# Performance work log

Measured on AMD Instinct MI355X. Metric: run time of the kernel, lower is better.

The kernel has to match this reference:

```python
import jax, jax.numpy as jnp
import numpy as np

B, C, H, W = 4, 512, 64, 64
CQ = C // 4  # query/key channels


def setup_inputs() -> dict:
    key = jax.random.key(0)
    ks = jax.random.split(key, 8)
    s_in = 1.0 / np.sqrt(C)
    return {
        "x": jax.random.normal(ks[0], (B, C, H, W), dtype=jnp.float32),
        "Wf_w": jax.random.normal(ks[1], (CQ, C), dtype=jnp.float32) * s_in,
        "Wf_b": jax.random.normal(ks[2], (CQ,), dtype=jnp.float32) * 0.01,
        "Wh_w": jax.random.normal(ks[3], (CQ, C), dtype=jnp.float32) * s_in,
        "Wh_b": jax.random.normal(ks[4], (CQ,), dtype=jnp.float32) * 0.01,
        "Wl_w": jax.random.normal(ks[5], (C, C), dtype=jnp.float32) * s_in,
        "Wl_b": jax.random.normal(ks[6], (C,), dtype=jnp.float32) * 0.01,
        "alpha": jax.random.uniform(ks[7], (1,), dtype=jnp.float32),
    }


def reference(x, Wf_w, Wf_b, Wh_w, Wh_b, Wl_w, Wl_b, alpha):
    b, c, h, w = x.shape
    n = h * w
    xr = x.reshape(b, c, n)  # (B, C, N)
    # 1x1 convs == per-pixel linear projections
    f = jnp.einsum('oc,bcn->bon', Wf_w, xr) + Wf_b[None, :, None]  # (B, C/4, N)
    k = jnp.einsum('oc,bcn->bon', Wh_w, xr) + Wh_b[None, :, None]  # (B, C/4, N)
    v = jnp.einsum('oc,bcn->bon', Wl_w, xr) + Wl_b[None, :, None]  # (B, C,   N)
    # t[b, i, j] = <f[:, i], k[:, j]>  -> (B, N, N)
    scores = jnp.einsum('boi,boj->bij', f, k)
    att = jax.nn.softmax(scores, axis=-1)
    # out[b, c, i] = sum_j v[b, c, j] * att[b, i, j]  (bmm with att^T)
    out = jnp.einsum('bcj,bij->bci', v, att)
    out = out.reshape(b, c, h, w)
    return out * alpha[0] + x
```

## Files before the change

### kernel.cpp

```cpp
#include <hip/hip_runtime.h>
#include <hip/hip_bf16.h>

typedef _Float16 f16;
typedef _Float16 f16x4 __attribute__((ext_vector_type(4)));
typedef _Float16 f16x8 __attribute__((ext_vector_type(8)));
typedef float f32x4 __attribute__((ext_vector_type(4)));

constexpr int BATCH = 4, C = 512, CQ = 128, N = 4096;
constexpr int OALL = 768;

constexpr size_t WS_FT   = 0;
constexpr size_t WS_KT   = WS_FT   + (size_t)BATCH * N * CQ * 2;
constexpr size_t WS_V    = WS_KT   + (size_t)BATCH * N * CQ * 2;
constexpr size_t WS_WALL = WS_V    + (size_t)BATCH * C * N * 2;
constexpr size_t WS_BALL = WS_WALL + (size_t)OALL * C * 2;

__global__ void prep_weights(const float* __restrict__ Wf_w, const float* __restrict__ Wf_b,
                             const float* __restrict__ Wh_w, const float* __restrict__ Wh_b,
                             const float* __restrict__ Wl_w, const float* __restrict__ Wl_b,
                             f16* __restrict__ wall, float* __restrict__ ball) {
    int i = blockIdx.x * 256 + threadIdx.x;
    if (i < OALL * C) {
        int o = i >> 9, c = i & 511;
        float v = (o < 128) ? Wf_w[o * C + c]
                : (o < 256) ? Wh_w[(o - 128) * C + c]
                            : Wl_w[(o - 256) * C + c];
        wall[i] = (f16)v;
    }
    if (i < OALL)
        ball[i] = (i < 128) ? Wf_b[i] : (i < 256) ? Wh_b[i - 128] : Wl_b[i - 256];
}

__global__ void __launch_bounds__(512) proj_all(const float* __restrict__ x, const f16* __restrict__ wall,
                                                const float* __restrict__ ball,
                                                f16* __restrict__ ft, f16* __restrict__ kt,
                                                f16* __restrict__ v) {
    __shared__ __align__(16) f16 xl[64][72];
    const int tid = threadIdx.x;
    const int wv  = tid >> 6;
    const int lane = tid & 63;
    const int li = lane & 15, lg = lane >> 4;
    const int b  = blockIdx.x >> 6;
    const int n0 = (blockIdx.x & 63) * 64;
    const int ob = wv * 96;
    const int nn = tid & 63, cg = tid >> 6;

    f32x4 acc[6][4] = {};
    for (int ch = 0; ch < 8; ++ch) {
        __syncthreads();
        {
            const float* xs = x + ((size_t)(b * C) + ch * 64 + cg * 8) * N + n0 + nn;
#pragma unroll
            for (int r = 0; r < 8; ++r)
                xl[nn][cg * 8 + r] = (f16)xs[(size_t)r * N];
        }
        __syncthreads();
#pragma unroll
        for (int ks = 0; ks < 2; ++ks) {
            f16x8 xfr[4];
#pragma unroll
            for (int nf = 0; nf < 4; ++nf)
                xfr[nf] = *(const f16x8*)(&xl[nf * 16 + li][ks * 32 + lg * 8]);
#pragma unroll
            for (int of = 0; of < 6; ++of) {
                f16x8 wfr = *(const f16x8*)(wall + (size_t)(ob + of * 16 + li) * C + ch * 64 + ks * 32 + lg * 8);
#pragma unroll
                for (int nf = 0; nf < 4; ++nf)
                    acc[of][nf] = __builtin_amdgcn_mfma_f32_16x16x32_f16(xfr[nf], wfr, acc[of][nf], 0, 0, 0);
            }
        }
    }
#pragma unroll
    for (int of = 0; of < 6; ++of) {
        const int o = ob + of * 16 + li;
        const float bias = ball[o];
#pragma unroll
        for (int nf = 0; nf < 4; ++nf)
#pragma unroll
            for (int r = 0; r < 4; ++r) {
                const int n = n0 + nf * 16 + lg * 4 + r;
                const f16 val = (f16)(acc[of][nf][r] + bias);
                if (o < 128) {
                    ft[(size_t)(b * N + n) * CQ + o] = val;
                } else if (o < 256) {
                    const int ck = o - 128;
                    kt[(((size_t)b * (N >> 2) + (n >> 2)) * 4 + (n & 3)) * 128 + ck] = val;
                } else {
                    const int c = o - 256;
                    v[(((size_t)b * 32 + (c >> 4)) * 512 + (n >> 3)) * 128 + (c & 15) * 8 + (n & 7)] = val;
                }
            }
    }
}

__global__ void __launch_bounds__(512, 2) attn(const f16* __restrict__ ft, const f16* __restrict__ kt,
                                               const f16* __restrict__ v,
                                               const float* __restrict__ x, const float* __restrict__ alphap,
                                               float* __restrict__ out) {
    __shared__ __align__(16) f16 kbuf[2][128 * 128];
    __shared__ __align__(16) f16 pbuf[64 * 128];
    __shared__ float smax[8][4][16];
    __shared__ float ssum[8][4][16];

    const int tid  = threadIdx.x;
    const int wv   = tid >> 6;
    const int lane = tid & 63;
    const int li = lane & 15, lg = lane >> 4;
    const int swl = li & 7;
    const int v0 = blockIdx.x;
    const int b  = (v0 & 7) >> 1;
    const int it = ((v0 & 1) << 5) | (v0 >> 3);
    const int i0 = it * 64;
    const int c0 = wv * 64;

    f16x8 fb[4][4];
#pragma unroll
    for (int f = 0; f < 4; ++f) {
        const f16* fp = ft + (size_t)(b * N + i0 + f * 16 + li) * CQ + lg * 8;
#pragma unroll
        for (int ks = 0; ks < 4; ++ks) fb[f][ks] = *(const f16x8*)(fp + ks * 32);
    }

    const f16* ktb = kt + (size_t)b * N * 128;
    {
#pragma unroll
        for (int k = 0; k < 4; ++k) {
            f16x8 vv = *(const f16x8*)(ktb + (((size_t)(wv * 4 + k)) * 4 + lg) * 128 + li * 8);
            *(f16x8*)(&kbuf[0][(wv * 16 + k * 4 + lg) * 128 + ((li ^ ((k * 4 + lg) & 7)) * 8)]) = vv;
        }
    }

    const f16* vb2 = v + (((size_t)b * 32 + wv * 4) * 512 + lg) * 128 + li * 8;
    f32x4 oacc[4][4] = {};
    float ms[4] = {-1e30f, -1e30f, -1e30f, -1e30f};
    float ls[4] = {0.f, 0.f, 0.f, 0.f};
    __syncthreads();

    for (int t = 0; t < 32; ++t) {
        const f16* kc = &kbuf[t & 1][0];
        f16*       kn = &kbuf[(t + 1) & 1][0];
        const size_t jb0 = (size_t)t * 16;
        const int gn = (t < 31) ? (t + 1) * 32 : 0;
        f16x8 stg[4];
#pragma unroll
        for (int k = 0; k < 4; ++k)
            stg[k] = *(const f16x8*)(ktb + (((size_t)(gn + wv * 4 + k)) * 4 + lg) * 128 + li * 8);

        f16x8 kf4[4];
#pragma unroll
        for (int ks = 0; ks < 4; ++ks)
            kf4[ks] = *(const f16x8*)(&kc[(wv * 16 + li) * 128 + ((ks * 4 + lg) ^ swl) * 8]);
        f32x4 s[4] = {};
        __builtin_amdgcn_s_setprio(1);
#pragma unroll
        for (int ks = 0; ks < 4; ++ks)
#pragma unroll
            for (int f = 0; f < 4; ++f)
                s[f] = __builtin_amdgcn_mfma_f32_16x16x32_f16(kf4[ks], fb[f][ks], s[f], 0, 0, 0);
        __builtin_amdgcn_s_setprio(0);

        float tm[4];
#pragma unroll
        for (int f = 0; f < 4; ++f) {
            float t0 = fmaxf(fmaxf(s[f][0], s[f][1]), fmaxf(s[f][2], s[f][3]));
            t0 = fmaxf(t0, __shfl_xor(t0, 16));
            t0 = fmaxf(t0, __shfl_xor(t0, 32));
            tm[f] = t0;
        }
        if (lane < 16) {
#pragma unroll
            for (int f = 0; f < 4; ++f) smax[wv][f][li] = tm[f];
        }
        f16x8 va[2][4];
#pragma unroll
        for (int cf = 0; cf < 4; ++cf) va[0][cf] = *(const f16x8*)(vb2 + ((size_t)cf * 512 + jb0) * 128);
        __syncthreads();
        float gm[4];
#pragma unroll
        for (int f = 0; f < 4; ++f) {
            float m0 = smax[0][f][li];
#pragma unroll
            for (int w = 1; w < 8; ++w) m0 = fmaxf(m0, smax[w][f][li]);
            gm[f] = m0;
        }
#pragma unroll
        for (int cf = 0; cf < 4; ++cf) va[1][cf] = *(const f16x8*)(vb2 + ((size_t)cf * 512 + jb0 + 4) * 128);
#pragma unroll
        for (int f = 0; f < 4; ++f) {
            if (!__all(gm[f] <= ms[f] + 8.0f)) {
                float mn = fmaxf(ms[f], gm[f]), sc = __expf(ms[f] - mn);
                ms[f] = mn; ls[f] *= sc;
#pragma unroll
                for (int cf = 0; cf < 4; ++cf) oacc[cf][f] *= sc;
            }
        }
        const int jl = wv * 16 + lg * 4;
        const int gg = (jl >> 3) ^ swl;
        float ps[4];
#pragma unroll
        for (int f = 0; f < 4; ++f) {
            f16x4 pk;
            float p0 = 0.f;
#pragma unroll
            for (int r = 0; r < 4; ++r) { float p = __expf(s[f][r] - ms[f]); p0 += p; pk[r] = (f16)p; }
            *(f16x4*)(&pbuf[(f * 16 + li) * 128 + gg * 8 + (jl & 7)]) = pk;
            ps[f] = p0;
        }
#pragma unroll
        for (int f = 0; f < 4; ++f) {
            ps[f] += __shfl_xor(ps[f], 16);
            ps[f] += __shfl_xor(ps[f], 32);
        }
        if (lane < 16) {
#pragma unroll
            for (int f = 0; f < 4; ++f) ssum[wv][f][li] = ps[f];
        }
#pragma unroll
        for (int k = 0; k < 4; ++k)
            *(f16x8*)(&kn[(wv * 16 + k * 4 + lg) * 128 + ((li ^ ((k * 4 + lg) & 7)) * 8)]) = stg[k];
        __syncthreads();
#pragma unroll
        for (int f = 0; f < 4; ++f) {
            float a0 = 0.f;
#pragma unroll
            for (int w = 0; w < 8; ++w) a0 += ssum[w][f][li];
            ls[f] += a0;
        }
#pragma unroll
        for (int kf = 0; kf < 4; ++kf) {
            const int cur = kf & 1;
            const int g = (kf * 4 + lg) ^ swl;
            f16x8 pb[4];
#pragma unroll
            for (int f = 0; f < 4; ++f)
                pb[f] = *(const f16x8*)(&pbuf[(f * 16 + li) * 128 + g * 8]);
            f16x8 vv0 = va[cur][0], vv1 = va[cur][1], vv2 = va[cur][2], vv3 = va[cur][3];
            if (kf < 2) {
#pragma unroll
                for (int cf = 0; cf < 4; ++cf)
                    va[cur][cf] = *(const f16x8*)(vb2 + ((size_t)cf * 512 + jb0 + (kf + 2) * 4) * 128);
            }
            __builtin_amdgcn_s_setprio(1);
#pragma unroll
            for (int f = 0; f < 4; ++f) {
                oacc[0][f] = __builtin_amdgcn_mfma_f32_16x16x32_f16(vv0, pb[f], oacc[0][f], 0, 0, 0);
                oacc[1][f] = __builtin_amdgcn_mfma_f32_16x16x32_f16(vv1, pb[f], oacc[1][f], 0, 0, 0);
                oacc[2][f] = __builtin_amdgcn_mfma_f32_16x16x32_f16(vv2, pb[f], oacc[2][f], 0, 0, 0);
                oacc[3][f] = __builtin_amdgcn_mfma_f32_16x16x32_f16(vv3, pb[f], oacc[3][f], 0, 0, 0);
            }
            __builtin_amdgcn_s_setprio(0);
        }
    }

    const float alpha = alphap[0];
#pragma unroll
    for (int f = 0; f < 4; ++f) {
        const float invf = alpha / ls[f];
        const float* xp = x + (size_t)(b * C + c0) * N + i0 + f * 16 + li;
        float* op = out + (size_t)(b * C + c0) * N + i0 + f * 16 + li;
#pragma unroll
        for (int cf = 0; cf < 4; ++cf)
#pragma unroll
            for (int r = 0; r < 4; ++r) {
                const int cl = cf * 16 + lg * 4 + r;
                op[(size_t)cl * N] = oacc[cf][f][r] * invf + xp[(size_t)cl * N];
            }
    }
}

extern "C" void kernel_launch(void* const* d_in, const int* in_sizes, int n_in,
                              void* d_out, int out_size, void* d_ws, size_t ws_size,
                              hipStream_t stream) {
    const float* x     = (const float*)d_in[0];
    const float* Wf_w  = (const float*)d_in[1];
    const float* Wf_b  = (const float*)d_in[2];
    const float* Wh_w  = (const float*)d_in[3];
    const float* Wh_b  = (const float*)d_in[4];
    const float* Wl_w  = (const float*)d_in[5];
    const float* Wl_b  = (const float*)d_in[6];
    const float* alpha = (const float*)d_in[7];
    char* ws = (char*)d_ws;
    f16*   ftb  = (f16*)(ws + WS_FT);
    f16*   ktb  = (f16*)(ws + WS_KT);
    f16*   vb   = (f16*)(ws + WS_V);
    f16*   wall = (f16*)(ws + WS_WALL);
    float* ball = (float*)(ws + WS_BALL);
    float* out  = (float*)d_out;

    prep_weights<<<dim3((OALL * C + 255) / 256), dim3(256), 0, stream>>>(Wf_w, Wf_b, Wh_w, Wh_b, Wl_w, Wl_b, wall, ball);
    proj_all<<<dim3(256), dim3(512), 0, stream>>>(x, wall, ball, ftb, ktb, vb);
    attn<<<dim3(256), dim3(512), 0, stream>>>(ftb, ktb, vb, x, alpha, out);
}
```

Baseline: 167.9 us.

## Load key fragments directly from global into registers, drop LDS key buffer

The attention kernel no longer stages key tiles through a double-buffered shared-memory buffer. Each wave now reads its own 16-row key fragment straight from global memory into registers and prefetches the next tile one iteration ahead. The projection kernel writes keys in a plain row-major layout to match. This removes 64KB of LDS per block, the LDS write/read traffic and one barrier, which could raise occupancy. The cost is more registers per thread and global key loads that are no longer shared through LDS.

```diff
diff --git a/kernel.cpp b/kernel.cpp
--- a/kernel.cpp
+++ b/kernel.cpp
@@ -84,7 +84,7 @@
                     ft[(size_t)(b * N + n) * CQ + o] = val;
                 } else if (o < 256) {
                     const int ck = o - 128;
-                    kt[(((size_t)b * (N >> 2) + (n >> 2)) * 4 + (n & 3)) * 128 + ck] = val;
+                    kt[((size_t)b * N + n) * 128 + ck] = val;
                 } else {
                     const int c = o - 256;
                     v[(((size_t)b * 32 + (c >> 4)) * 512 + (n >> 3)) * 128 + (c & 15) * 8 + (n & 7)] = val;
@@ -97,7 +97,6 @@
                                                const f16* __restrict__ v,
                                                const float* __restrict__ x, const float* __restrict__ alphap,
                                                float* __restrict__ out) {
-    __shared__ __align__(16) f16 kbuf[2][128 * 128];
     __shared__ __align__(16) f16 pbuf[64 * 128];
     __shared__ float smax[8][4][16];
     __shared__ float ssum[8][4][16];
@@ -121,42 +120,30 @@
         for (int ks = 0; ks < 4; ++ks) fb[f][ks] = *(const f16x8*)(fp + ks * 32);
     }
 
-    const f16* ktb = kt + (size_t)b * N * 128;
-    {
-#pragma unroll
-        for (int k = 0; k < 4; ++k) {
-            f16x8 vv = *(const f16x8*)(ktb + (((size_t)(wv * 4 + k)) * 4 + lg) * 128 + li * 8);
-            *(f16x8*)(&kbuf[0][(wv * 16 + k * 4 + lg) * 128 + ((li ^ ((k * 4 + lg) & 7)) * 8)]) = vv;
-        }
-    }
+    const f16* kL = kt + ((size_t)b * N + wv * 16 + li) * 128 + lg * 8;
+    f16x8 kf[4];
+#pragma unroll
+    for (int ks = 0; ks < 4; ++ks) kf[ks] = *(const f16x8*)(kL + ks * 32);
 
     const f16* vb2 = v + (((size_t)b * 32 + wv * 4) * 512 + lg) * 128 + li * 8;
     f32x4 oacc[4][4] = {};
     float ms[4] = {-1e30f, -1e30f, -1e30f, -1e30f};
     float ls[4] = {0.f, 0.f, 0.f, 0.f};
-    __syncthreads();
 
     for (int t = 0; t < 32; ++t) {
-        const f16* kc = &kbuf[t & 1][0];
-        f16*       kn = &kbuf[(t + 1) & 1][0];
         const size_t jb0 = (size_t)t * 16;
-        const int gn = (t < 31) ? (t + 1) * 32 : 0;
-        f16x8 stg[4];
-#pragma unroll
-        for (int k = 0; k < 4; ++k)
-            stg[k] = *(const f16x8*)(ktb + (((size_t)(gn + wv * 4 + k)) * 4 + lg) * 128 + li * 8);
-
-        f16x8 kf4[4];
-#pragma unroll
-        for (int ks = 0; ks < 4; ++ks)
-            kf4[ks] = *(const f16x8*)(&kc[(wv * 16 + li) * 128 + ((ks * 4 + lg) ^ swl) * 8]);
+        f16x8 kfn[4];
+        const size_t knext = (size_t)((t < 31) ? (t + 1) : 0) * 128 * 128;
+#pragma unroll
+        for (int ks = 0; ks < 4; ++ks) kfn[ks] = *(const f16x8*)(kL + knext + ks * 32);
+
         f32x4 s[4] = {};
         __builtin_amdgcn_s_setprio(1);
 #pragma unroll
         for (int ks = 0; ks < 4; ++ks)
 #pragma unroll
             for (int f = 0; f < 4; ++f)
-                s[f] = __builtin_amdgcn_mfma_f32_16x16x32_f16(kf4[ks], fb[f][ks], s[f], 0, 0, 0);
+                s[f] = __builtin_amdgcn_mfma_f32_16x16x32_f16(kf[ks], fb[f][ks], s[f], 0, 0, 0);
         __builtin_amdgcn_s_setprio(0);
 
         float tm[4];
@@ -215,9 +202,6 @@
 #pragma unroll
             for (int f = 0; f < 4; ++f) ssum[wv][f][li] = ps[f];
         }
-#pragma unroll
-        for (int k = 0; k < 4; ++k)
-            *(f16x8*)(&kn[(wv * 16 + k * 4 + lg) * 128 + ((li ^ ((k * 4 + lg) & 7)) * 8)]) = stg[k];
         __syncthreads();
 #pragma unroll
         for (int f = 0; f < 4; ++f) {
@@ -227,18 +211,18 @@
             ls[f] += a0;
         }
 #pragma unroll
-        for (int kf = 0; kf < 4; ++kf) {
-            const int cur = kf & 1;
-            const int g = (kf * 4 + lg) ^ swl;
+        for (int kf2 = 0; kf2 < 4; ++kf2) {
+            const int cur = kf2 & 1;
+            const int g = (kf2 * 4 + lg) ^ swl;
             f16x8 pb[4];
 #pragma unroll
             for (int f = 0; f < 4; ++f)
                 pb[f] = *(const f16x8*)(&pbuf[(f * 16 + li) * 128 + g * 8]);
             f16x8 vv0 = va[cur][0], vv1 = va[cur][1], vv2 = va[cur][2], vv3 = va[cur][3];
-            if (kf < 2) {
+            if (kf2 < 2) {
 #pragma unroll
                 for (int cf = 0; cf < 4; ++cf)
-                    va[cur][cf] = *(const f16x8*)(vb2 + ((size_t)cf * 512 + jb0 + (kf + 2) * 4) * 128);
+                    va[cur][cf] = *(const f16x8*)(vb2 + ((size_t)cf * 512 + jb0 + (kf2 + 2) * 4) * 128);
             }
             __builtin_amdgcn_s_setprio(1);
 #pragma unroll
@@ -250,6 +234,8 @@
             }
             __builtin_amdgcn_s_setprio(0);
         }
+#pragma unroll
+        for (int ks = 0; ks < 4; ++ks) kf[ks] = kfn[ks];
     }
 
     const float alpha = alphap[0];
```

New measurement: 160.5 us. 1.05x faster.
